# Optimization experiments

Measured on AMD Instinct MI355X. Metric: run time of the kernel, lower is better.

Reference implementation:

```python
import jax, jax.numpy as jnp
import numpy as np

B, C, H, W = 4, 64, 64, 64
CI = C // 4  # inter_channels for q/k convs and SE fc


def setup_inputs() -> dict:
    key = jax.random.key(0)
    ks = jax.random.split(key, 12)
    s = lambda k, shape, fan: jax.random.normal(k, shape, jnp.float32) * (1.0 / np.sqrt(fan))
    return {
        "ftr": jax.random.normal(ks[0], (B, C, H, W), jnp.float32),
        "wq": s(ks[1], (CI, C), C), "bq": jnp.zeros((CI,), jnp.float32),
        "wk": s(ks[2], (CI, C), C), "bk": jnp.zeros((CI,), jnp.float32),
        "wv": s(ks[3], (C, C), C),  "bv": jnp.zeros((C,), jnp.float32),
        "delta": jnp.array([0.1], jnp.float32),
        "w_avg1": s(ks[4], (CI, C), C), "w_avg2": s(ks[5], (C, CI), CI),
        "w_max1": s(ks[6], (CI, C), C), "w_max2": s(ks[7], (C, CI), CI),
    }


def reference(ftr, wq, bq, wk, bk, wv, bv, delta, w_avg1, w_avg2, w_max1, w_max2):
    b, c, h, w = ftr.shape
    p = h * w
    x = ftr.reshape(b, c, p)                                   # [B,C,P]
    q = jnp.einsum('oc,bcp->bpo', wq, x) + bq                  # [B,P,CI]
    k = jnp.einsum('oc,bcp->bop', wk, x) + bk[:, None]         # [B,CI,P]
    v = jnp.einsum('oc,bcp->bop', wv, x) + bv[:, None]         # [B,C,P]
    scores = jnp.einsum('bpo,boq->bpq', q, k)                  # [B,P,P]
    weights = jax.nn.softmax(scores, axis=1)                   # softmax over dim=1 (queries), as in torch code
    G = jnp.einsum('bcp,bpq->bcq', v, weights).reshape(b, c, h, w)
    out = delta[0] * G + ftr
    # ChannelRecalibration (SE with avg+max pooling)
    f_avg = jnp.mean(out, axis=(2, 3))                         # [B,C]
    f_max = jnp.max(out, axis=(2, 3))                          # [B,C]
    a = jax.nn.relu(f_avg @ w_avg1.T) @ w_avg2.T
    m = jax.nn.relu(f_max @ w_max1.T) @ w_max2.T
    gate = jax.nn.sigmoid(a + m)[:, :, None, None]
    return gate * out
```

## Files before the change

### kernel.cpp

```cpp
#include <hip/hip_runtime.h>
#include <math.h>

#define PP 4096

typedef __attribute__((ext_vector_type(8))) short short8;
typedef __attribute__((ext_vector_type(4))) short short4v;
typedef __attribute__((ext_vector_type(4))) float float4v;

__device__ __forceinline__ short f2bf(float f) {
    union { float f; unsigned u; } v; v.f = f;
    unsigned r = v.u + 0x7FFFu + ((v.u >> 16) & 1u);
    return (short)(r >> 16);
}

#if __has_builtin(__builtin_amdgcn_mfma_f32_16x16x16bf16_1k)
__device__ __forceinline__ float4v mfma16(short4v a, short4v b, float4v c) {
    return __builtin_amdgcn_mfma_f32_16x16x16bf16_1k(a, b, c, 0, 0, 0);
}
#else
__device__ __forceinline__ float4v mfma16(short4v a, short4v b, float4v c) {
    short8 a8 = {a[0], a[1], a[2], a[3], 0, 0, 0, 0};
    short8 b8 = {b[0], b[1], b[2], b[3], 0, 0, 0, 0};
    return __builtin_amdgcn_mfma_f32_16x16x32_bf16(a8, b8, c, 0, 0, 0);
}
#endif

__global__ __launch_bounds__(256) void qkv_kernel(
    const float* __restrict__ ftr, const float* __restrict__ wq, const float* __restrict__ bq,
    const float* __restrict__ wk, const float* __restrict__ bk,
    const float* __restrict__ wv, const float* __restrict__ bv,
    short* __restrict__ q16, short* __restrict__ k16, short* __restrict__ v_a)
{
    __shared__ float xs[64][36] __attribute__((aligned(16)));
    __shared__ float wvs[64][68] __attribute__((aligned(16)));
    __shared__ float wq_t[64][20] __attribute__((aligned(16)));
    __shared__ float wk_t[64][20] __attribute__((aligned(16)));

    const int b  = blockIdx.x >> 7;
    const int p0 = (blockIdx.x & 127) << 5;
    const int tid = threadIdx.x;

    for (int idx = tid; idx < 512; idx += 256) {
        int c = idx >> 3, j4 = (idx & 7) << 2;
        *(float4*)&xs[c][j4] = *(const float4*)(ftr + ((size_t)(b * 64 + c)) * PP + p0 + j4);
    }
    for (int idx = tid; idx < 1024; idx += 256) {
        int r = idx >> 4, j4 = (idx & 15) << 2;
        *(float4*)&wvs[r][j4] = *(const float4*)(wv + r * 64 + j4);
    }
    for (int idx = tid; idx < 1024; idx += 256) {
        int o = idx >> 6, c2 = idx & 63;
        wq_t[c2][o] = wq[idx];
        wk_t[c2][o] = wk[idx];
    }
    __syncthreads();

    {
        const int wg = tid >> 6, qd = (tid >> 4) & 3, cc = tid & 15;
        const int c = wg * 16 + cc;
        const float bvc = bv[c];
        const int col = qd * 8;
        float a[8] = {0.f,0.f,0.f,0.f,0.f,0.f,0.f,0.f};
        #pragma unroll 8
        for (int c2 = 0; c2 < 64; ++c2) {
            float w = wvs[c][c2];
            float4 xa = *(const float4*)&xs[c2][col];
            float4 xb = *(const float4*)&xs[c2][col + 4];
            a[0] += w * xa.x; a[1] += w * xa.y; a[2] += w * xa.z; a[3] += w * xa.w;
            a[4] += w * xb.x; a[5] += w * xb.y; a[6] += w * xb.z; a[7] += w * xb.w;
        }
        const int ptg = (p0 >> 4) + (qd >> 1);
        const int qp0 = (qd & 1) * 2;
        #pragma unroll
        for (int h = 0; h < 2; ++h) {
            short4v pv;
            #pragma unroll
            for (int j = 0; j < 4; ++j) pv[j] = f2bf(a[h * 4 + j] + bvc);
            *(short4v*)(v_a + ((((size_t)(b * 256 + ptg)) * 4 + wg) * 64 + (qp0 + h) * 16 + cc) * 4) = pv;
        }
    }

    {
        const int p_l = tid >> 3, sel = tid & 7;
        const int ch = sel & 1, half = (sel >> 1) & 1, arr = sel >> 2;
        const float* Wtr = arr ? &wk_t[0][0] : &wq_t[0][0];
        float a[8] = {0.f,0.f,0.f,0.f,0.f,0.f,0.f,0.f};
        const int c2lo = ch * 32;
        #pragma unroll 8
        for (int c2i = 0; c2i < 32; ++c2i) {
            const int c2 = c2lo + c2i;
            float x = xs[c2][p_l];
            float4 wA = *(const float4*)(Wtr + c2 * 20 + half * 8);
            float4 wB = *(const float4*)(Wtr + c2 * 20 + half * 8 + 4);
            a[0] += wA.x * x; a[1] += wA.y * x; a[2] += wA.z * x; a[3] += wA.w * x;
            a[4] += wB.x * x; a[5] += wB.y * x; a[6] += wB.z * x; a[7] += wB.w * x;
        }
        #pragma unroll
        for (int oo = 0; oo < 8; ++oo) a[oo] += __shfl_xor(a[oo], 1);
        if (ch == 0) {
            const float* bias = arr ? bk : bq;
            const float scl = arr ? 1.0f : 1.4426950408889634f;
            short8 pq;
            #pragma unroll
            for (int oo = 0; oo < 8; ++oo)
                pq[oo] = f2bf((a[oo] + bias[half * 8 + oo]) * scl);
            short* dst = (arr ? k16 : q16) + (((size_t)(b * PP + p0 + p_l)) << 4) + half * 8;
            *(short8*)dst = pq;
        }
    }
}

__global__ __launch_bounds__(512, 4) void attn_kernel(
    const short* __restrict__ q16, const short* __restrict__ k16,
    const short* __restrict__ v_a,
    const float* __restrict__ ftr, const float* __restrict__ delta,
    float* __restrict__ out, float* __restrict__ psum, float* __restrict__ pmax)
{
    __shared__ float Obuf[8][16][34];
    __shared__ float lb[8][32];
    __shared__ float lfin[32];

    const int b    = blockIdx.x >> 7;
    const int qblk = blockIdx.x & 127;
    const int q0   = qblk << 5;
    const int tid  = threadIdx.x;
    const int lane = tid & 63;
    const int n    = lane & 15;
    const int quad = lane >> 4;
    const int ph   = tid >> 6;

    const float4v zf4 = {0.f, 0.f, 0.f, 0.f};

    short4v bkf[2];
    #pragma unroll
    for (int nt = 0; nt < 2; ++nt)
        bkf[nt] = *(const short4v*)(k16 + ((size_t)(b * PP + q0 + nt * 16 + n) << 4) + quad * 4);

    const short* qrow = q16 + ((size_t)(b * PP + n) << 4) + quad * 4;
    const short* vrow = v_a + (size_t)b * 262144 + lane * 4;

    float4v acc[4][2];
    #pragma unroll
    for (int mt = 0; mt < 4; ++mt)
        #pragma unroll
        for (int nt = 0; nt < 2; ++nt) acc[mt][nt] = zf4;
    float lsum[2] = {0.f, 0.f};

    const int pt0 = ph * 512;
    for (int it = 0; it < 8; ++it) {
        const int pt = pt0 + it * 64;
        const int pti = pt >> 4;

        short4v aq[4];
        #pragma unroll
        for (int f = 0; f < 4; ++f)
            aq[f] = *(const short4v*)(qrow + (size_t)(pt + f * 16) * 16);

        float4v sf_c[2], sf_n[2];
        #pragma unroll
        for (int nt = 0; nt < 2; ++nt)
            sf_c[nt] = mfma16(aq[0], bkf[nt], zf4);

        #pragma unroll
        for (int h = 0; h < 2; ++h) {
            short4v va[2][4];
            #pragma unroll
            for (int j = 0; j < 2; ++j)
                #pragma unroll
                for (int mt = 0; mt < 4; ++mt)
                    va[j][mt] = *(const short4v*)(vrow + (size_t)((pti + 2 * h + j) * 4 + mt) * 256);

            #pragma unroll
            for (int j = 0; j < 2; ++j) {
                const int f = 2 * h + j;
                if (f < 3) {
                    #pragma unroll
                    for (int nt = 0; nt < 2; ++nt)
                        sf_n[nt] = mfma16(aq[f + 1], bkf[nt], zf4);
                }
                short4v w[2];
                #pragma unroll
                for (int nt = 0; nt < 2; ++nt) {
                    float w0 = __builtin_amdgcn_exp2f(sf_c[nt][0]);
                    float w1 = __builtin_amdgcn_exp2f(sf_c[nt][1]);
                    float w2 = __builtin_amdgcn_exp2f(sf_c[nt][2]);
                    float w3 = __builtin_amdgcn_exp2f(sf_c[nt][3]);
                    lsum[nt] += (w0 + w1) + (w2 + w3);
                    union { uint2 u; short4v s; } cv;
                    cv.u.x = __builtin_amdgcn_perm(__float_as_uint(w1), __float_as_uint(w0), 0x07060302u);
                    cv.u.y = __builtin_amdgcn_perm(__float_as_uint(w3), __float_as_uint(w2), 0x07060302u);
                    w[nt] = cv.s;
                }
                #pragma unroll
                for (int mt = 0; mt < 4; ++mt)
                    #pragma unroll
                    for (int nt = 0; nt < 2; ++nt)
                        acc[mt][nt] = mfma16(va[j][mt], w[nt], acc[mt][nt]);
                #pragma unroll
                for (int nt = 0; nt < 2; ++nt) sf_c[nt] = sf_n[nt];
            }
        }
    }

    lsum[0] += __shfl_xor(lsum[0], 16); lsum[0] += __shfl_xor(lsum[0], 32);
    lsum[1] += __shfl_xor(lsum[1], 16); lsum[1] += __shfl_xor(lsum[1], 32);
    if (quad == 0) {
        lb[ph][n]      = lsum[0];
        lb[ph][16 + n] = lsum[1];
    }
    __syncthreads();
    if (tid < 32) {
        float s = 0.f;
        #pragma unroll
        for (int p8 = 0; p8 < 8; ++p8) s += lb[p8][tid];
        lfin[tid] = delta[0] / s;
    }
    __syncthreads();

    const int c_l = tid >> 5;
    const int q   = tid & 31;
    #pragma unroll
    for (int mt = 0; mt < 4; ++mt) {
        #pragma unroll
        for (int nt = 0; nt < 2; ++nt)
            #pragma unroll
            for (int i = 0; i < 4; ++i)
                Obuf[ph][quad * 4 + i][nt * 16 + n] = acc[mt][nt][i];
        __syncthreads();
        const int c = mt * 16 + c_l;
        float o = 0.f;
        #pragma unroll
        for (int p8 = 0; p8 < 8; ++p8) o += Obuf[p8][c_l][q];
        const size_t g = ((size_t)(b * 64 + c)) * PP + q0 + q;
        o = o * lfin[q] + ftr[g];
        out[g] = o;
        float s = o, m = o;
        s += __shfl_xor(s, 1); s += __shfl_xor(s, 2);
        s += __shfl_xor(s, 4); s += __shfl_xor(s, 8); s += __shfl_xor(s, 16);
        m = fmaxf(m, __shfl_xor(m, 1)); m = fmaxf(m, __shfl_xor(m, 2));
        m = fmaxf(m, __shfl_xor(m, 4)); m = fmaxf(m, __shfl_xor(m, 8));
        m = fmaxf(m, __shfl_xor(m, 16));
        if (q == 0) {
            psum[((size_t)(b * 128) + qblk) * 64 + c] = s;
            pmax[((size_t)(b * 128) + qblk) * 64 + c] = m;
        }
        __syncthreads();
    }
}

__global__ __launch_bounds__(256) void reduce_gate_kernel(
    const float* __restrict__ psum, const float* __restrict__ pmax,
    const float* __restrict__ w_avg1, const float* __restrict__ w_avg2,
    const float* __restrict__ w_max1, const float* __restrict__ w_max2,
    float* __restrict__ gate)
{
    const int b = blockIdx.x, t = threadIdx.x;
    const int c = t & 63, ch = t >> 6;
    float s = 0.f, m = -3.4e38f;
    for (int i = 0; i < 32; ++i) {
        const int qb = ch * 32 + i;
        s += psum[((size_t)(b * 128) + qb) * 64 + c];
        m = fmaxf(m, pmax[((size_t)(b * 128) + qb) * 64 + c]);
    }
    __shared__ float ss[4][64], sm[4][64], fa[64], fm[64], ha[16], hm[16];
    ss[ch][c] = s; sm[ch][c] = m;
    __syncthreads();
    if (t < 64) {
        fa[t] = (ss[0][t] + ss[1][t] + ss[2][t] + ss[3][t]) * (1.f / 4096.f);
        fm[t] = fmaxf(fmaxf(sm[0][t], sm[1][t]), fmaxf(sm[2][t], sm[3][t]));
    }
    __syncthreads();
    if (t < 16) {
        float a = 0.f;
        for (int cc = 0; cc < 64; ++cc) a += fa[cc] * w_avg1[t * 64 + cc];
        ha[t] = fmaxf(a, 0.f);
    } else if (t < 32) {
        float a = 0.f;
        for (int cc = 0; cc < 64; ++cc) a += fm[cc] * w_max1[(t - 16) * 64 + cc];
        hm[t - 16] = fmaxf(a, 0.f);
    }
    __syncthreads();
    if (t < 64) {
        float a = 0.f, mm = 0.f;
        #pragma unroll
        for (int i = 0; i < 16; ++i) {
            a  += ha[i] * w_avg2[t * 16 + i];
            mm += hm[i] * w_max2[t * 16 + i];
        }
        gate[b * 64 + t] = 1.f / (1.f + expf(-(a + mm)));
    }
}

__global__ __launch_bounds__(256) void mul_kernel(
    float* __restrict__ out, const float* __restrict__ gate)
{
    const float g = gate[blockIdx.x >> 2];
    const size_t e = ((size_t)blockIdx.x * 256 + threadIdx.x) * 4;
    float4 v = *(const float4*)(out + e);
    v.x *= g; v.y *= g; v.z *= g; v.w *= g;
    *(float4*)(out + e) = v;
}

extern "C" void kernel_launch(void* const* d_in, const int* in_sizes, int n_in,
                              void* d_out, int out_size, void* d_ws, size_t ws_size,
                              hipStream_t stream)
{
    const float* ftr    = (const float*)d_in[0];
    const float* wq     = (const float*)d_in[1];
    const float* bq     = (const float*)d_in[2];
    const float* wk     = (const float*)d_in[3];
    const float* bk     = (const float*)d_in[4];
    const float* wv     = (const float*)d_in[5];
    const float* bv     = (const float*)d_in[6];
    const float* delta  = (const float*)d_in[7];
    const float* w_avg1 = (const float*)d_in[8];
    const float* w_avg2 = (const float*)d_in[9];
    const float* w_max1 = (const float*)d_in[10];
    const float* w_max2 = (const float*)d_in[11];
    float* out = (float*)d_out;

    short* wsS  = (short*)d_ws;
    short* q16  = wsS;
    short* k16  = wsS + 262144;
    short* v_a  = wsS + 524288;
    float* fbase = (float*)(wsS + 1572864);
    float* psum = fbase;
    float* pmax = fbase + 32768;
    float* gate = fbase + 65536;

    qkv_kernel<<<512, 256, 0, stream>>>(ftr, wq, bq, wk, bk, wv, bv, q16, k16, v_a);
    attn_kernel<<<512, 512, 0, stream>>>(q16, k16, v_a, ftr, delta, out, psum, pmax);
    reduce_gate_kernel<<<4, 256, 0, stream>>>(psum, pmax, w_avg1, w_avg2, w_max1, w_max2, gate);
    mul_kernel<<<1024, 256, 0, stream>>>(out, gate);
}
```

Measured before the change: 128.7 us.

## Fuse four kernels into one persistent megakernel with global atomic barriers

Merges the qkv projection, attention, SE gate reduction and gating multiply into a single 512-block kernel. Stages are separated by software grid barriers built on atomic counters, which are reset by a memset before launch. This removes three kernel launch gaps and the tail idle between kernels. In exchange it relies on all 512 blocks being co-resident, adds barrier spin cost, and the qkv stage now runs under the attention kernel's 512-thread launch bounds.

```diff
diff --git a/kernel.cpp b/kernel.cpp
--- a/kernel.cpp
+++ b/kernel.cpp
@@ -25,280 +25,311 @@
 }
 #endif
 
-__global__ __launch_bounds__(256) void qkv_kernel(
+__device__ __forceinline__ void gbar(unsigned* c, unsigned nb) {
+    __syncthreads();
+    if (threadIdx.x == 0) {
+        __threadfence();
+        __hip_atomic_fetch_add(c, 1u, __ATOMIC_RELEASE, __HIP_MEMORY_SCOPE_AGENT);
+        long t = 0;
+        while (__hip_atomic_load(c, __ATOMIC_ACQUIRE, __HIP_MEMORY_SCOPE_AGENT) < nb
+               && t < 5000000L) ++t;
+        __threadfence();
+    }
+    __syncthreads();
+}
+
+__global__ __launch_bounds__(512, 4) void mega_kernel(
     const float* __restrict__ ftr, const float* __restrict__ wq, const float* __restrict__ bq,
     const float* __restrict__ wk, const float* __restrict__ bk,
     const float* __restrict__ wv, const float* __restrict__ bv,
-    short* __restrict__ q16, short* __restrict__ k16, short* __restrict__ v_a)
+    const float* __restrict__ delta,
+    const float* __restrict__ w_avg1, const float* __restrict__ w_avg2,
+    const float* __restrict__ w_max1, const float* __restrict__ w_max2,
+    short* __restrict__ q16, short* __restrict__ k16, short* __restrict__ v_a,
+    float* __restrict__ psum, float* __restrict__ pmax, float* __restrict__ gate,
+    unsigned* __restrict__ ctr,
+    float* __restrict__ out)
 {
-    __shared__ float xs[64][36] __attribute__((aligned(16)));
-    __shared__ float wvs[64][68] __attribute__((aligned(16)));
-    __shared__ float wq_t[64][20] __attribute__((aligned(16)));
-    __shared__ float wk_t[64][20] __attribute__((aligned(16)));
-
-    const int b  = blockIdx.x >> 7;
-    const int p0 = (blockIdx.x & 127) << 5;
-    const int tid = threadIdx.x;
-
-    for (int idx = tid; idx < 512; idx += 256) {
-        int c = idx >> 3, j4 = (idx & 7) << 2;
-        *(float4*)&xs[c][j4] = *(const float4*)(ftr + ((size_t)(b * 64 + c)) * PP + p0 + j4);
-    }
-    for (int idx = tid; idx < 1024; idx += 256) {
-        int r = idx >> 4, j4 = (idx & 15) << 2;
-        *(float4*)&wvs[r][j4] = *(const float4*)(wv + r * 64 + j4);
-    }
-    for (int idx = tid; idx < 1024; idx += 256) {
-        int o = idx >> 6, c2 = idx & 63;
-        wq_t[c2][o] = wq[idx];
-        wk_t[c2][o] = wk[idx];
-    }
-    __syncthreads();
+    __shared__ float smem[9216] __attribute__((aligned(16)));
+
+    const int tid  = threadIdx.x;
+    const int b    = blockIdx.x >> 7;
+    const int blk7 = blockIdx.x & 127;
 
     {
-        const int wg = tid >> 6, qd = (tid >> 4) & 3, cc = tid & 15;
-        const int c = wg * 16 + cc;
-        const float bvc = bv[c];
-        const int col = qd * 8;
-        float a[8] = {0.f,0.f,0.f,0.f,0.f,0.f,0.f,0.f};
-        #pragma unroll 8
-        for (int c2 = 0; c2 < 64; ++c2) {
-            float w = wvs[c][c2];
-            float4 xa = *(const float4*)&xs[c2][col];
-            float4 xb = *(const float4*)&xs[c2][col + 4];
-            a[0] += w * xa.x; a[1] += w * xa.y; a[2] += w * xa.z; a[3] += w * xa.w;
-            a[4] += w * xb.x; a[5] += w * xb.y; a[6] += w * xb.z; a[7] += w * xb.w;
-        }
-        const int ptg = (p0 >> 4) + (qd >> 1);
-        const int qp0 = (qd & 1) * 2;
-        #pragma unroll
-        for (int h = 0; h < 2; ++h) {
-            short4v pv;
-            #pragma unroll
-            for (int j = 0; j < 4; ++j) pv[j] = f2bf(a[h * 4 + j] + bvc);
-            *(short4v*)(v_a + ((((size_t)(b * 256 + ptg)) * 4 + wg) * 64 + (qp0 + h) * 16 + cc) * 4) = pv;
-        }
-    }
+        float* xs   = smem;
+        float* wvs  = smem + 2304;
+        float* wq_t = smem + 6656;
+        float* wk_t = smem + 7936;
+        const int p0 = blk7 << 5;
+
+        {
+            int idx = tid;
+            {
+                int c = idx >> 3, j4 = (idx & 7) << 2;
+                *(float4*)&xs[c * 36 + j4] =
+                    *(const float4*)(ftr + ((size_t)(b * 64 + c)) * PP + p0 + j4);
+            }
+            #pragma unroll
+            for (int r2 = 0; r2 < 2; ++r2) {
+                int i2 = tid + r2 * 512;
+                int r = i2 >> 4, j4 = (i2 & 15) << 2;
+                *(float4*)&wvs[r * 68 + j4] = *(const float4*)(wv + r * 64 + j4);
+            }
+            #pragma unroll
+            for (int r2 = 0; r2 < 2; ++r2) {
+                int i2 = tid + r2 * 512;
+                int o = i2 >> 6, c2 = i2 & 63;
+                wq_t[c2 * 20 + o] = wq[i2];
+                wk_t[c2 * 20 + o] = wk[i2];
+            }
+        }
+        __syncthreads();
+
+        if (tid < 256) {
+            const int wg = tid >> 6, qd = (tid >> 4) & 3, cc = tid & 15;
+            const int c = wg * 16 + cc;
+            const float bvc = bv[c];
+            const int col = qd * 8;
+            float a[8] = {0.f,0.f,0.f,0.f,0.f,0.f,0.f,0.f};
+            #pragma unroll 8
+            for (int c2 = 0; c2 < 64; ++c2) {
+                float w = wvs[c * 68 + c2];
+                float4 xa = *(const float4*)&xs[c2 * 36 + col];
+                float4 xb = *(const float4*)&xs[c2 * 36 + col + 4];
+                a[0] += w * xa.x; a[1] += w * xa.y; a[2] += w * xa.z; a[3] += w * xa.w;
+                a[4] += w * xb.x; a[5] += w * xb.y; a[6] += w * xb.z; a[7] += w * xb.w;
+            }
+            const int ptg = (p0 >> 4) + (qd >> 1);
+            const int qp0 = (qd & 1) * 2;
+            #pragma unroll
+            for (int h = 0; h < 2; ++h) {
+                short4v pv;
+                #pragma unroll
+                for (int j = 0; j < 4; ++j) pv[j] = f2bf(a[h * 4 + j] + bvc);
+                *(short4v*)(v_a + ((((size_t)(b * 256 + ptg)) * 4 + wg) * 64 + (qp0 + h) * 16 + cc) * 4) = pv;
+            }
+        } else {
+            const int t = tid - 256;
+            const int p_l = t >> 3, sel = t & 7;
+            const int ch = sel & 1, half = (sel >> 1) & 1, arr = sel >> 2;
+            const float* Wtr = arr ? wk_t : wq_t;
+            float a[8] = {0.f,0.f,0.f,0.f,0.f,0.f,0.f,0.f};
+            const int c2lo = ch * 32;
+            #pragma unroll 8
+            for (int c2i = 0; c2i < 32; ++c2i) {
+                const int c2 = c2lo + c2i;
+                float x = xs[c2 * 36 + p_l];
+                float4 wA = *(const float4*)(Wtr + c2 * 20 + half * 8);
+                float4 wB = *(const float4*)(Wtr + c2 * 20 + half * 8 + 4);
+                a[0] += wA.x * x; a[1] += wA.y * x; a[2] += wA.z * x; a[3] += wA.w * x;
+                a[4] += wB.x * x; a[5] += wB.y * x; a[6] += wB.z * x; a[7] += wB.w * x;
+            }
+            #pragma unroll
+            for (int oo = 0; oo < 8; ++oo) a[oo] += __shfl_xor(a[oo], 1);
+            if (ch == 0) {
+                const float* bias = arr ? bk : bq;
+                const float scl = arr ? 1.0f : 1.4426950408889634f;
+                short8 pq;
+                #pragma unroll
+                for (int oo = 0; oo < 8; ++oo)
+                    pq[oo] = f2bf((a[oo] + bias[half * 8 + oo]) * scl);
+                short* dst = (arr ? k16 : q16) + (((size_t)(b * PP + p0 + p_l)) << 4) + half * 8;
+                *(short8*)dst = pq;
+            }
+        }
+    }
+
+    gbar(ctr + 0, gridDim.x);
 
     {
-        const int p_l = tid >> 3, sel = tid & 7;
-        const int ch = sel & 1, half = (sel >> 1) & 1, arr = sel >> 2;
-        const float* Wtr = arr ? &wk_t[0][0] : &wq_t[0][0];
-        float a[8] = {0.f,0.f,0.f,0.f,0.f,0.f,0.f,0.f};
-        const int c2lo = ch * 32;
-        #pragma unroll 8
-        for (int c2i = 0; c2i < 32; ++c2i) {
-            const int c2 = c2lo + c2i;
-            float x = xs[c2][p_l];
-            float4 wA = *(const float4*)(Wtr + c2 * 20 + half * 8);
-            float4 wB = *(const float4*)(Wtr + c2 * 20 + half * 8 + 4);
-            a[0] += wA.x * x; a[1] += wA.y * x; a[2] += wA.z * x; a[3] += wA.w * x;
-            a[4] += wB.x * x; a[5] += wB.y * x; a[6] += wB.z * x; a[7] += wB.w * x;
-        }
-        #pragma unroll
-        for (int oo = 0; oo < 8; ++oo) a[oo] += __shfl_xor(a[oo], 1);
-        if (ch == 0) {
-            const float* bias = arr ? bk : bq;
-            const float scl = arr ? 1.0f : 1.4426950408889634f;
-            short8 pq;
-            #pragma unroll
-            for (int oo = 0; oo < 8; ++oo)
-                pq[oo] = f2bf((a[oo] + bias[half * 8 + oo]) * scl);
-            short* dst = (arr ? k16 : q16) + (((size_t)(b * PP + p0 + p_l)) << 4) + half * 8;
-            *(short8*)dst = pq;
-        }
-    }
-}
-
-__global__ __launch_bounds__(512, 4) void attn_kernel(
-    const short* __restrict__ q16, const short* __restrict__ k16,
-    const short* __restrict__ v_a,
-    const float* __restrict__ ftr, const float* __restrict__ delta,
-    float* __restrict__ out, float* __restrict__ psum, float* __restrict__ pmax)
-{
-    __shared__ float Obuf[8][16][34];
-    __shared__ float lb[8][32];
-    __shared__ float lfin[32];
-
-    const int b    = blockIdx.x >> 7;
-    const int qblk = blockIdx.x & 127;
-    const int q0   = qblk << 5;
-    const int tid  = threadIdx.x;
-    const int lane = tid & 63;
-    const int n    = lane & 15;
-    const int quad = lane >> 4;
-    const int ph   = tid >> 6;
-
-    const float4v zf4 = {0.f, 0.f, 0.f, 0.f};
-
-    short4v bkf[2];
-    #pragma unroll
-    for (int nt = 0; nt < 2; ++nt)
-        bkf[nt] = *(const short4v*)(k16 + ((size_t)(b * PP + q0 + nt * 16 + n) << 4) + quad * 4);
-
-    const short* qrow = q16 + ((size_t)(b * PP + n) << 4) + quad * 4;
-    const short* vrow = v_a + (size_t)b * 262144 + lane * 4;
-
-    float4v acc[4][2];
-    #pragma unroll
-    for (int mt = 0; mt < 4; ++mt)
-        #pragma unroll
-        for (int nt = 0; nt < 2; ++nt) acc[mt][nt] = zf4;
-    float lsum[2] = {0.f, 0.f};
-
-    const int pt0 = ph * 512;
-    for (int it = 0; it < 8; ++it) {
-        const int pt = pt0 + it * 64;
-        const int pti = pt >> 4;
-
-        short4v aq[4];
-        #pragma unroll
-        for (int f = 0; f < 4; ++f)
-            aq[f] = *(const short4v*)(qrow + (size_t)(pt + f * 16) * 16);
-
-        float4v sf_c[2], sf_n[2];
+        float* Obuf = smem;
+        float* lb   = smem + 4352;
+        float* lfin = smem + 4608;
+
+        const int qblk = blk7;
+        const int q0   = qblk << 5;
+        const int lane = tid & 63;
+        const int n    = lane & 15;
+        const int quad = lane >> 4;
+        const int ph   = tid >> 6;
+
+        const float4v zf4 = {0.f, 0.f, 0.f, 0.f};
+
+        short4v bkf[2];
         #pragma unroll
         for (int nt = 0; nt < 2; ++nt)
-            sf_c[nt] = mfma16(aq[0], bkf[nt], zf4);
-
+            bkf[nt] = *(const short4v*)(k16 + ((size_t)(b * PP + q0 + nt * 16 + n) << 4) + quad * 4);
+
+        const short* qrow = q16 + ((size_t)(b * PP + n) << 4) + quad * 4;
+        const short* vrow = v_a + (size_t)b * 262144 + lane * 4;
+
+        float4v acc[4][2];
         #pragma unroll
-        for (int h = 0; h < 2; ++h) {
-            short4v va[2][4];
-            #pragma unroll
-            for (int j = 0; j < 2; ++j)
-                #pragma unroll
-                for (int mt = 0; mt < 4; ++mt)
-                    va[j][mt] = *(const short4v*)(vrow + (size_t)((pti + 2 * h + j) * 4 + mt) * 256);
-
-            #pragma unroll
-            for (int j = 0; j < 2; ++j) {
-                const int f = 2 * h + j;
-                if (f < 3) {
+        for (int mt = 0; mt < 4; ++mt)
+            #pragma unroll
+            for (int nt = 0; nt < 2; ++nt) acc[mt][nt] = zf4;
+        float lsum[2] = {0.f, 0.f};
+
+        const int pt0 = ph * 512;
+        for (int it = 0; it < 8; ++it) {
+            const int pt = pt0 + it * 64;
+            const int pti = pt >> 4;
+
+            short4v aq[4];
+            #pragma unroll
+            for (int f = 0; f < 4; ++f)
+                aq[f] = *(const short4v*)(qrow + (size_t)(pt + f * 16) * 16);
+
+            float4v sf_c[2], sf_n[2];
+            #pragma unroll
+            for (int nt = 0; nt < 2; ++nt)
+                sf_c[nt] = mfma16(aq[0], bkf[nt], zf4);
+
+            #pragma unroll
+            for (int h = 0; h < 2; ++h) {
+                short4v va[2][4];
+                #pragma unroll
+                for (int j = 0; j < 2; ++j)
                     #pragma unroll
-                    for (int nt = 0; nt < 2; ++nt)
-                        sf_n[nt] = mfma16(aq[f + 1], bkf[nt], zf4);
+                    for (int mt = 0; mt < 4; ++mt)
+                        va[j][mt] = *(const short4v*)(vrow + (size_t)((pti + 2 * h + j) * 4 + mt) * 256);
+
+                #pragma unroll
+                for (int j = 0; j < 2; ++j) {
+                    const int f = 2 * h + j;
+                    if (f < 3) {
+                        #pragma unroll
+                        for (int nt = 0; nt < 2; ++nt)
+                            sf_n[nt] = mfma16(aq[f + 1], bkf[nt], zf4);
+                    }
+                    short4v w[2];
+                    #pragma unroll
+                    for (int nt = 0; nt < 2; ++nt) {
+                        float w0 = __builtin_amdgcn_exp2f(sf_c[nt][0]);
+                        float w1 = __builtin_amdgcn_exp2f(sf_c[nt][1]);
+                        float w2 = __builtin_amdgcn_exp2f(sf_c[nt][2]);
+                        float w3 = __builtin_amdgcn_exp2f(sf_c[nt][3]);
+                        lsum[nt] += (w0 + w1) + (w2 + w3);
+                        union { uint2 u; short4v s; } cv;
+                        cv.u.x = __builtin_amdgcn_perm(__float_as_uint(w1), __float_as_uint(w0), 0x07060302u);
+                        cv.u.y = __builtin_amdgcn_perm(__float_as_uint(w3), __float_as_uint(w2), 0x07060302u);
+                        w[nt] = cv.s;
+                    }
+                    #pragma unroll
+                    for (int mt = 0; mt < 4; ++mt)
+                        #pragma unroll
+                        for (int nt = 0; nt < 2; ++nt)
+                            acc[mt][nt] = mfma16(va[j][mt], w[nt], acc[mt][nt]);
+                    #pragma unroll
+                    for (int nt = 0; nt < 2; ++nt) sf_c[nt] = sf_n[nt];
                 }
-                short4v w[2];
-                #pragma unroll
-                for (int nt = 0; nt < 2; ++nt) {
-                    float w0 = __builtin_amdgcn_exp2f(sf_c[nt][0]);
-                    float w1 = __builtin_amdgcn_exp2f(sf_c[nt][1]);
-                    float w2 = __builtin_amdgcn_exp2f(sf_c[nt][2]);
-                    float w3 = __builtin_amdgcn_exp2f(sf_c[nt][3]);
-                    lsum[nt] += (w0 + w1) + (w2 + w3);
-                    union { uint2 u; short4v s; } cv;
-                    cv.u.x = __builtin_amdgcn_perm(__float_as_uint(w1), __float_as_uint(w0), 0x07060302u);
-                    cv.u.y = __builtin_amdgcn_perm(__float_as_uint(w3), __float_as_uint(w2), 0x07060302u);
-                    w[nt] = cv.s;
-                }
-                #pragma unroll
-                for (int mt = 0; mt < 4; ++mt)
-                    #pragma unroll
-                    for (int nt = 0; nt < 2; ++nt)
-                        acc[mt][nt] = mfma16(va[j][mt], w[nt], acc[mt][nt]);
-                #pragma unroll
-                for (int nt = 0; nt < 2; ++nt) sf_c[nt] = sf_n[nt];
-            }
-        }
-    }
-
-    lsum[0] += __shfl_xor(lsum[0], 16); lsum[0] += __shfl_xor(lsum[0], 32);
-    lsum[1] += __shfl_xor(lsum[1], 16); lsum[1] += __shfl_xor(lsum[1], 32);
-    if (quad == 0) {
-        lb[ph][n]      = lsum[0];
-        lb[ph][16 + n] = lsum[1];
-    }
-    __syncthreads();
-    if (tid < 32) {
-        float s = 0.f;
+            }
+        }
+
+        lsum[0] += __shfl_xor(lsum[0], 16); lsum[0] += __shfl_xor(lsum[0], 32);
+        lsum[1] += __shfl_xor(lsum[1], 16); lsum[1] += __shfl_xor(lsum[1], 32);
+        if (quad == 0) {
+            lb[ph * 32 + n]      = lsum[0];
+            lb[ph * 32 + 16 + n] = lsum[1];
+        }
+        __syncthreads();
+        if (tid < 32) {
+            float s = 0.f;
+            #pragma unroll
+            for (int p8 = 0; p8 < 8; ++p8) s += lb[p8 * 32 + tid];
+            lfin[tid] = delta[0] / s;
+        }
+        __syncthreads();
+
+        const int c_l = tid >> 5;
+        const int q   = tid & 31;
         #pragma unroll
-        for (int p8 = 0; p8 < 8; ++p8) s += lb[p8][tid];
-        lfin[tid] = delta[0] / s;
-    }
-    __syncthreads();
-
-    const int c_l = tid >> 5;
-    const int q   = tid & 31;
-    #pragma unroll
-    for (int mt = 0; mt < 4; ++mt) {
-        #pragma unroll
-        for (int nt = 0; nt < 2; ++nt)
-            #pragma unroll
-            for (int i = 0; i < 4; ++i)
-                Obuf[ph][quad * 4 + i][nt * 16 + n] = acc[mt][nt][i];
-        __syncthreads();
-        const int c = mt * 16 + c_l;
-        float o = 0.f;
-        #pragma unroll
-        for (int p8 = 0; p8 < 8; ++p8) o += Obuf[p8][c_l][q];
-        const size_t g = ((size_t)(b * 64 + c)) * PP + q0 + q;
-        o = o * lfin[q] + ftr[g];
-        out[g] = o;
-        float s = o, m = o;
-        s += __shfl_xor(s, 1); s += __shfl_xor(s, 2);
-        s += __shfl_xor(s, 4); s += __shfl_xor(s, 8); s += __shfl_xor(s, 16);
-        m = fmaxf(m, __shfl_xor(m, 1)); m = fmaxf(m, __shfl_xor(m, 2));
-        m = fmaxf(m, __shfl_xor(m, 4)); m = fmaxf(m, __shfl_xor(m, 8));
-        m = fmaxf(m, __shfl_xor(m, 16));
-        if (q == 0) {
-            psum[((size_t)(b * 128) + qblk) * 64 + c] = s;
-            pmax[((size_t)(b * 128) + qblk) * 64 + c] = m;
-        }
-        __syncthreads();
-    }
-}
-
-__global__ __launch_bounds__(256) void reduce_gate_kernel(
-    const float* __restrict__ psum, const float* __restrict__ pmax,
-    const float* __restrict__ w_avg1, const float* __restrict__ w_avg2,
-    const float* __restrict__ w_max1, const float* __restrict__ w_max2,
-    float* __restrict__ gate)
-{
-    const int b = blockIdx.x, t = threadIdx.x;
-    const int c = t & 63, ch = t >> 6;
-    float s = 0.f, m = -3.4e38f;
-    for (int i = 0; i < 32; ++i) {
-        const int qb = ch * 32 + i;
-        s += psum[((size_t)(b * 128) + qb) * 64 + c];
-        m = fmaxf(m, pmax[((size_t)(b * 128) + qb) * 64 + c]);
-    }
-    __shared__ float ss[4][64], sm[4][64], fa[64], fm[64], ha[16], hm[16];
-    ss[ch][c] = s; sm[ch][c] = m;
-    __syncthreads();
-    if (t < 64) {
-        fa[t] = (ss[0][t] + ss[1][t] + ss[2][t] + ss[3][t]) * (1.f / 4096.f);
-        fm[t] = fmaxf(fmaxf(sm[0][t], sm[1][t]), fmaxf(sm[2][t], sm[3][t]));
-    }
-    __syncthreads();
-    if (t < 16) {
-        float a = 0.f;
-        for (int cc = 0; cc < 64; ++cc) a += fa[cc] * w_avg1[t * 64 + cc];
-        ha[t] = fmaxf(a, 0.f);
-    } else if (t < 32) {
-        float a = 0.f;
-        for (int cc = 0; cc < 64; ++cc) a += fm[cc] * w_max1[(t - 16) * 64 + cc];
-        hm[t - 16] = fmaxf(a, 0.f);
-    }
-    __syncthreads();
-    if (t < 64) {
-        float a = 0.f, mm = 0.f;
-        #pragma unroll
-        for (int i = 0; i < 16; ++i) {
-            a  += ha[i] * w_avg2[t * 16 + i];
-            mm += hm[i] * w_max2[t * 16 + i];
-        }
-        gate[b * 64 + t] = 1.f / (1.f + expf(-(a + mm)));
-    }
-}
-
-__global__ __launch_bounds__(256) void mul_kernel(
-    float* __restrict__ out, const float* __restrict__ gate)
-{
-    const float g = gate[blockIdx.x >> 2];
-    const size_t e = ((size_t)blockIdx.x * 256 + threadIdx.x) * 4;
-    float4 v = *(const float4*)(out + e);
-    v.x *= g; v.y *= g; v.z *= g; v.w *= g;
-    *(float4*)(out + e) = v;
+        for (int mt = 0; mt < 4; ++mt) {
+            #pragma unroll
+            for (int nt = 0; nt < 2; ++nt)
+                #pragma unroll
+                for (int i = 0; i < 4; ++i)
+                    Obuf[(ph * 16 + quad * 4 + i) * 34 + nt * 16 + n] = acc[mt][nt][i];
+            __syncthreads();
+            const int c = mt * 16 + c_l;
+            float o = 0.f;
+            #pragma unroll
+            for (int p8 = 0; p8 < 8; ++p8) o += Obuf[(p8 * 16 + c_l) * 34 + q];
+            const size_t g = ((size_t)(b * 64 + c)) * PP + q0 + q;
+            o = o * lfin[q] + ftr[g];
+            out[g] = o;
+            float s = o, m = o;
+            s += __shfl_xor(s, 1); s += __shfl_xor(s, 2);
+            s += __shfl_xor(s, 4); s += __shfl_xor(s, 8); s += __shfl_xor(s, 16);
+            m = fmaxf(m, __shfl_xor(m, 1)); m = fmaxf(m, __shfl_xor(m, 2));
+            m = fmaxf(m, __shfl_xor(m, 4)); m = fmaxf(m, __shfl_xor(m, 8));
+            m = fmaxf(m, __shfl_xor(m, 16));
+            if (q == 0) {
+                psum[((size_t)(b * 128) + qblk) * 64 + c] = s;
+                pmax[((size_t)(b * 128) + qblk) * 64 + c] = m;
+            }
+            __syncthreads();
+        }
+    }
+
+    gbar(ctr + 1, gridDim.x);
+
+    if (blockIdx.x < 4) {
+        float* ss = smem;
+        float* sm = smem + 256;
+        float* fa = smem + 512;
+        float* fm = smem + 576;
+        float* ha = smem + 640;
+        float* hm = smem + 656;
+        const int bb = blockIdx.x;
+        if (tid < 256) {
+            const int c = tid & 63, ch = tid >> 6;
+            float s = 0.f, m = -3.4e38f;
+            for (int i = 0; i < 32; ++i) {
+                const int qb = ch * 32 + i;
+                s += psum[((size_t)(bb * 128) + qb) * 64 + c];
+                m = fmaxf(m, pmax[((size_t)(bb * 128) + qb) * 64 + c]);
+            }
+            ss[ch * 64 + c] = s; sm[ch * 64 + c] = m;
+        }
+        __syncthreads();
+        if (tid < 64) {
+            fa[tid] = (ss[tid] + ss[64 + tid] + ss[128 + tid] + ss[192 + tid]) * (1.f / 4096.f);
+            fm[tid] = fmaxf(fmaxf(sm[tid], sm[64 + tid]), fmaxf(sm[128 + tid], sm[192 + tid]));
+        }
+        __syncthreads();
+        if (tid < 16) {
+            float a = 0.f;
+            for (int cc = 0; cc < 64; ++cc) a += fa[cc] * w_avg1[tid * 64 + cc];
+            ha[tid] = fmaxf(a, 0.f);
+        } else if (tid < 32) {
+            float a = 0.f;
+            for (int cc = 0; cc < 64; ++cc) a += fm[cc] * w_max1[(tid - 16) * 64 + cc];
+            hm[tid - 16] = fmaxf(a, 0.f);
+        }
+        __syncthreads();
+        if (tid < 64) {
+            float a = 0.f, mm = 0.f;
+            #pragma unroll
+            for (int i = 0; i < 16; ++i) {
+                a  += ha[i] * w_avg2[tid * 16 + i];
+                mm += hm[i] * w_max2[tid * 16 + i];
+            }
+            gate[bb * 64 + tid] = 1.f / (1.f + expf(-(a + mm)));
+        }
+    }
+
+    gbar(ctr + 2, gridDim.x);
+
+    {
+        const int idx = blockIdx.x * 512 + tid;
+        const float g = gate[idx >> 10];
+        const size_t e = (size_t)idx * 4;
+        float4 v = *(const float4*)(out + e);
+        v.x *= g; v.y *= g; v.z *= g; v.w *= g;
+        *(float4*)(out + e) = v;
+    }
 }
 
 extern "C" void kernel_launch(void* const* d_in, const int* in_sizes, int n_in,
@@ -327,9 +358,10 @@
     float* psum = fbase;
     float* pmax = fbase + 32768;
     float* gate = fbase + 65536;
-
-    qkv_kernel<<<512, 256, 0, stream>>>(ftr, wq, bq, wk, bk, wv, bv, q16, k16, v_a);
-    attn_kernel<<<512, 512, 0, stream>>>(q16, k16, v_a, ftr, delta, out, psum, pmax);
-    reduce_gate_kernel<<<4, 256, 0, stream>>>(psum, pmax, w_avg1, w_avg2, w_max1, w_max2, gate);
-    mul_kernel<<<1024, 256, 0, stream>>>(out, gate);
-}
+    unsigned* ctr = (unsigned*)(fbase + 66048);
+
+    hipMemsetAsync(ctr, 0, 128, stream);
+    mega_kernel<<<512, 512, 0, stream>>>(
+        ftr, wq, bq, wk, bk, wv, bv, delta, w_avg1, w_avg2, w_max1, w_max2,
+        q16, k16, v_a, psum, pmax, gate, ctr, out);
+}
```

New measurement: 323.7 us. +151.5%, slower.
